# Optimization experiments

Hardware: AMD Instinct MI355X
Metric: run time of the kernel (lower is better)

Reference implementation:

```python
import jax, jax.numpy as jnp
import numpy as np

N = 1024      # num_features
H = 256       # num_hidden_features
E = 64        # embedding_size
HD = 64       # hidden_size
B = 8192


def setup_inputs() -> dict:
    key = jax.random.key(0)
    ks = jax.random.split(key, 7)
    glorot_e = (2.0 / (N + E)) ** 0.5
    glorot_w = (2.0 / (2 * E + HD)) ** 0.5
    glorot_u = (2.0 / (HD + 1)) ** 0.5
    return {
        "values": jax.random.uniform(ks[0], (B, N), dtype=jnp.float32),
        "feat_emb": jax.random.normal(ks[1], (N, E), dtype=jnp.float32) * glorot_e,
        "hid_emb": jax.random.normal(ks[2], (H, E), dtype=jnp.float32) * glorot_e,
        "W_w": jax.random.normal(ks[3], (2 * E, HD), dtype=jnp.float32) * glorot_w,
        "b_w": jnp.zeros((HD,), dtype=jnp.float32),
        "W_u": jax.random.normal(ks[4], (HD, 1), dtype=jnp.float32) * glorot_u,
        "mask": jax.random.bernoulli(ks[5], 0.5, (N, N + H)),
    }


def _forward(values, feat_emb, hid_emb, W_w, b_w, W_u, mask):
    # full embedding table over extended vocab: [M, E], M = N + H
    full = jnp.concatenate([feat_emb, hid_emb], axis=0)
    # Dense w applied to concat([feat_i, full_j]) == split-matmul, avoids [N,M,2E]
    W1, W2 = W_w[:E], W_w[E:]                      # each [E, HD]
    a = feat_emb @ W1                              # [N, HD]
    b = full @ W2                                  # [M, HD]
    h = jnp.tanh(a[:, None, :] + b[None, :, :] + b_w)  # [N, M, HD]
    score = jnp.squeeze(h @ W_u, axis=-1)          # [N, M]
    score = jnp.where(mask, jnp.exp(score), 0.0)
    score_sum = jnp.sum(score, axis=1, keepdims=True)
    score_sum = jnp.where(score_sum == 0, 1.0, score_sum)
    attention_weights = score / score_sum          # [N, M]
    context = attention_weights @ full             # [N, E]
    return values @ context                        # [B, E]


def reference(values, feat_emb, hid_emb, W_w, b_w, W_u, mask):
    return _forward(values, feat_emb, hid_emb, W_w, b_w, W_u, mask)
```

## Files before the change

kernel.cpp:

```cpp
#include <hip/hip_runtime.h>
#include <hip/hip_bf16.h>

#define NF   1024
#define NHID 256
#define NJ   1280
#define ED   64
#define BATCH 8192
#define SCB  320

#if defined(__has_builtin) && __has_builtin(__builtin_amdgcn_exp2f)
#define EXP2(x) __builtin_amdgcn_exp2f(x)
#else
#define EXP2(x) exp2f(x)
#endif
#define K2E 2.8853900817779268f

__global__ __launch_bounds__(256) void prep_kernel(
    const float* __restrict__ feat, const float* __restrict__ hid,
    const float* __restrict__ Ww, const float* __restrict__ bw,
    float* __restrict__ A, float* __restrict__ BvT)
{
    __shared__ float tile[32][65];
    const int tid = threadIdx.x;
    const int e   = tid & 63;
    const int wv  = tid >> 6;
    const int r0  = blockIdx.x * 32;
    const bool isA = (r0 < NF);
    const float* W = isA ? Ww : (Ww + 64 * 64);

    float wcol[64];
    #pragma unroll
    for (int k = 0; k < 64; k++) wcol[k] = W[k * 64 + e];
    const float bias = isA ? 0.f : bw[e];

    #pragma unroll
    for (int rr = 0; rr < 8; rr++) {
        int r  = r0 + wv * 8 + rr;
        int jf = isA ? r : (r - NF);
        jf = __builtin_amdgcn_readfirstlane(jf);
        const float* in = (jf < NF) ? (feat + (size_t)jf * 64)
                                    : (hid  + (size_t)(jf - NF) * 64);
        float a0 = 0.f, a1 = 0.f, a2 = 0.f, a3 = 0.f;
        #pragma unroll
        for (int k4 = 0; k4 < 64; k4 += 16) {
            float4 q0 = *(const float4*)(in + k4);
            float4 q1 = *(const float4*)(in + k4 + 4);
            float4 q2 = *(const float4*)(in + k4 + 8);
            float4 q3 = *(const float4*)(in + k4 + 12);
            a0 += q0.x*wcol[k4+0] + q0.y*wcol[k4+1] + q0.z*wcol[k4+2] + q0.w*wcol[k4+3];
            a1 += q1.x*wcol[k4+4] + q1.y*wcol[k4+5] + q1.z*wcol[k4+6] + q1.w*wcol[k4+7];
            a2 += q2.x*wcol[k4+8] + q2.y*wcol[k4+9] + q2.z*wcol[k4+10]+ q2.w*wcol[k4+11];
            a3 += q3.x*wcol[k4+12]+ q3.y*wcol[k4+13]+ q3.z*wcol[k4+14]+ q3.w*wcol[k4+15];
        }
        float res = (a0 + a1) + (a2 + a3) + bias;
        if (isA) A[(size_t)r * 64 + e] = res;
        else     tile[wv * 8 + rr][e] = res;
    }
    if (!isA) {
        __syncthreads();
        const int j0 = r0 - NF;
        const int ee = tid >> 2;
        #pragma unroll
        for (int h = 0; h < 2; h++) {
            int c = (tid & 3) + h * 4;
            float4 v;
            v.x = tile[c * 4 + 0][ee];
            v.y = tile[c * 4 + 1][ee];
            v.z = tile[c * 4 + 2][ee];
            v.w = tile[c * 4 + 3][ee];
            *(float4*)&BvT[(size_t)ee * NJ + j0 + c * 4] = v;
        }
    }
}

__global__ __launch_bounds__(SCB) void score_ctx_kernel(
    const float* __restrict__ feat, const float* __restrict__ hid,
    const float* __restrict__ Wu, const float* __restrict__ A,
    const float* __restrict__ BvT, const void* __restrict__ maskp,
    float* __restrict__ ctx)
{
    __shared__ __align__(16) float4 sPack[64];
    __shared__ __align__(16) float sc0[NJ], sc1[NJ];
    __shared__ __align__(16) float red[2][20][64];
    __shared__ float wpart[2][5];
    __shared__ float ssum[2];
    __shared__ float sSwu;
    __shared__ int   mtype_s;

    const int tid = threadIdx.x;
    const int i0  = blockIdx.x * 2;

    if (tid < 64) {
        const unsigned int* mw = (const unsigned int*)maskp;
        unsigned int w = mw[tid];
        unsigned long long notf = __ballot(w != 0u && w != 0x3F800000u);
        unsigned long long gt1  = __ballot(w > 1u);
        if (tid == 0) mtype_s = (notf == 0ull) ? 2 : ((gt1 == 0ull) ? 1 : 0);
        float wu = Wu[tid];
        float4 p;
        p.x = A[(size_t)i0 * 64 + tid];
        p.y = A[(size_t)(i0 + 1) * 64 + tid];
        p.z = wu; p.w = 0.f;
        sPack[tid] = p;
        float s = wu;
        #pragma unroll
        for (int off = 32; off > 0; off >>= 1) s += __shfl_down(s, off);
        if (tid == 0) sSwu = s;
    }
    __syncthreads();

    const int j4 = tid * 4;
    float4 acc0 = {0.f,0.f,0.f,0.f};
    float4 acc1 = {0.f,0.f,0.f,0.f};
    #pragma unroll 4
    for (int e = 0; e < 64; e++) {
        float4 b = *(const float4*)(BvT + (size_t)e * NJ + j4);
        float4 p = sPack[e];
        float x, r;
        x = p.x + b.x; r = __builtin_amdgcn_rcpf(EXP2(x * K2E) + 1.f); acc0.x = fmaf(p.z, r, acc0.x);
        x = p.x + b.y; r = __builtin_amdgcn_rcpf(EXP2(x * K2E) + 1.f); acc0.y = fmaf(p.z, r, acc0.y);
        x = p.x + b.z; r = __builtin_amdgcn_rcpf(EXP2(x * K2E) + 1.f); acc0.z = fmaf(p.z, r, acc0.z);
        x = p.x + b.w; r = __builtin_amdgcn_rcpf(EXP2(x * K2E) + 1.f); acc0.w = fmaf(p.z, r, acc0.w);
        x = p.y + b.x; r = __builtin_amdgcn_rcpf(EXP2(x * K2E) + 1.f); acc1.x = fmaf(p.z, r, acc1.x);
        x = p.y + b.y; r = __builtin_amdgcn_rcpf(EXP2(x * K2E) + 1.f); acc1.y = fmaf(p.z, r, acc1.y);
        x = p.y + b.z; r = __builtin_amdgcn_rcpf(EXP2(x * K2E) + 1.f); acc1.z = fmaf(p.z, r, acc1.z);
        x = p.y + b.w; r = __builtin_amdgcn_rcpf(EXP2(x * K2E) + 1.f); acc1.w = fmaf(p.z, r, acc1.w);
    }
    const float Swu = sSwu;
    const int mtype = mtype_s;
    const unsigned char* m8  = (const unsigned char*)maskp;
    const unsigned int*  m32 = (const unsigned int*)maskp;
    const float*         mfl = (const float*)maskp;
    bool b00,b01,b02,b03, b10,b11,b12,b13;
    if (mtype == 0) {
        unsigned m0 = *(const unsigned*)(m8 + (size_t)i0 * NJ + j4);
        unsigned m1 = *(const unsigned*)(m8 + (size_t)(i0+1) * NJ + j4);
        b00 = m0 & 0xffu; b01 = m0 & 0xff00u; b02 = m0 & 0xff0000u; b03 = m0 & 0xff000000u;
        b10 = m1 & 0xffu; b11 = m1 & 0xff00u; b12 = m1 & 0xff0000u; b13 = m1 & 0xff000000u;
    } else if (mtype == 1) {
        uint4 m0 = *(const uint4*)(m32 + (size_t)i0 * NJ + j4);
        uint4 m1 = *(const uint4*)(m32 + (size_t)(i0+1) * NJ + j4);
        b00 = m0.x; b01 = m0.y; b02 = m0.z; b03 = m0.w;
        b10 = m1.x; b11 = m1.y; b12 = m1.z; b13 = m1.w;
    } else {
        float4 m0 = *(const float4*)(mfl + (size_t)i0 * NJ + j4);
        float4 m1 = *(const float4*)(mfl + (size_t)(i0+1) * NJ + j4);
        b00 = m0.x != 0.f; b01 = m0.y != 0.f; b02 = m0.z != 0.f; b03 = m0.w != 0.f;
        b10 = m1.x != 0.f; b11 = m1.y != 0.f; b12 = m1.z != 0.f; b13 = m1.w != 0.f;
    }
    float4 e0, e1;
    e0.x = b00 ? __expf(Swu - 2.f*acc0.x) : 0.f;
    e0.y = b01 ? __expf(Swu - 2.f*acc0.y) : 0.f;
    e0.z = b02 ? __expf(Swu - 2.f*acc0.z) : 0.f;
    e0.w = b03 ? __expf(Swu - 2.f*acc0.w) : 0.f;
    e1.x = b10 ? __expf(Swu - 2.f*acc1.x) : 0.f;
    e1.y = b11 ? __expf(Swu - 2.f*acc1.y) : 0.f;
    e1.z = b12 ? __expf(Swu - 2.f*acc1.z) : 0.f;
    e1.w = b13 ? __expf(Swu - 2.f*acc1.w) : 0.f;
    *(float4*)&sc0[j4] = e0;
    *(float4*)&sc1[j4] = e1;
    float lsum0 = (e0.x + e0.y) + (e0.z + e0.w);
    float lsum1 = (e1.x + e1.y) + (e1.z + e1.w);
    #pragma unroll
    for (int off = 32; off > 0; off >>= 1) {
        lsum0 += __shfl_down(lsum0, off);
        lsum1 += __shfl_down(lsum1, off);
    }
    if ((tid & 63) == 0) { wpart[0][tid >> 6] = lsum0; wpart[1][tid >> 6] = lsum1; }
    __syncthreads();
    if (tid < 2) {
        float s = wpart[tid][0] + wpart[tid][1] + wpart[tid][2] + wpart[tid][3] + wpart[tid][4];
        ssum[tid] = (s == 0.f) ? 1.f : s;
    }
    __syncthreads();

    const int jg = tid >> 4;
    const int e4 = (tid & 15) * 4;
    float4 c0 = {0.f,0.f,0.f,0.f}, c1 = {0.f,0.f,0.f,0.f};
    for (int it = 0; it < 64; it++) {
        int j = it * 20 + jg;
        const float* fr = (j < NF) ? (feat + (size_t)j * 64)
                                   : (hid  + (size_t)(j - NF) * 64);
        float4 f = *(const float4*)(fr + e4);
        float w0 = sc0[j], w1 = sc1[j];
        c0.x += w0*f.x; c0.y += w0*f.y; c0.z += w0*f.z; c0.w += w0*f.w;
        c1.x += w1*f.x; c1.y += w1*f.y; c1.z += w1*f.z; c1.w += w1*f.w;
    }
    *(float4*)&red[0][jg][e4] = c0;
    *(float4*)&red[1][jg][e4] = c1;
    __syncthreads();
    if (tid < 128) {
        int half = tid >> 6, e = tid & 63;
        float v = 0.f;
        #pragma unroll
        for (int g = 0; g < 20; g++) v += red[half][g][e];
        ctx[(size_t)(i0 + half) * 64 + e] = v / ssum[half];
    }
}

__global__ __launch_bounds__(256) void out_mm_kernel(
    const float* __restrict__ values, const float* __restrict__ ctxp,
    float* __restrict__ dst, int atomic_mode)
{
    __shared__ __align__(16) float vsT[64 * 64];
    __shared__ __align__(16) float cs[64][64];
    const int tid = threadIdx.x;
    const int rt  = blockIdx.x >> 2;
    const int kq  = blockIdx.x & 3;
    const int r0  = rt * 64;
    const int tr  = tid >> 4;
    const int tc4 = (tid & 15) * 4;

    float acc[4][4];
    #pragma unroll
    for (int a = 0; a < 4; a++)
        #pragma unroll
        for (int b = 0; b < 4; b++) acc[a][b] = 0.f;

    for (int ch = 0; ch < 4; ch++) {
        const int k0 = kq * 256 + ch * 64;
        __syncthreads();
        #pragma unroll
        for (int s = 0; s < 4; s++) {
            int t   = tid + s * 256;
            int r   = t >> 4;
            int kk4 = (t & 15) * 4;
            float4 g = *(const float4*)&values[(size_t)(r0 + r) * NF + k0 + kk4];
            int p  = (((r >> 2) + (t & 15)) & 15) * 4 + (r & 3);
            vsT[(kk4 + 0) * 64 + p] = g.x;
            vsT[(kk4 + 1) * 64 + p] = g.y;
            vsT[(kk4 + 2) * 64 + p] = g.z;
            vsT[(kk4 + 3) * 64 + p] = g.w;
        }
        #pragma unroll
        for (int s = 0; s < 4; s++) {
            int t  = tid + s * 256;
            int kk = t >> 4;
            int c4 = (t & 15) * 4;
            *(float4*)&cs[kk][c4] = *(const float4*)&ctxp[(size_t)(k0 + kk) * ED + c4];
        }
        __syncthreads();
        #pragma unroll 8
        for (int k = 0; k < 64; k++) {
            float4 av = *(const float4*)&vsT[k * 64 + (((tr + (k >> 2)) & 15) << 2)];
            float4 bv = *(const float4*)&cs[k][tc4];
            acc[0][0] += av.x*bv.x; acc[0][1] += av.x*bv.y; acc[0][2] += av.x*bv.z; acc[0][3] += av.x*bv.w;
            acc[1][0] += av.y*bv.x; acc[1][1] += av.y*bv.y; acc[1][2] += av.y*bv.z; acc[1][3] += av.y*bv.w;
            acc[2][0] += av.z*bv.x; acc[2][1] += av.z*bv.y; acc[2][2] += av.z*bv.z; acc[2][3] += av.z*bv.w;
            acc[3][0] += av.w*bv.x; acc[3][1] += av.w*bv.y; acc[3][2] += av.w*bv.z; acc[3][3] += av.w*bv.w;
        }
    }
    if (atomic_mode) {
        #pragma unroll
        for (int i2 = 0; i2 < 4; i2++) {
            int r = r0 + tr * 4 + i2;
            float* op = dst + (size_t)r * ED + tc4;
            unsafeAtomicAdd(op + 0, acc[i2][0]);
            unsafeAtomicAdd(op + 1, acc[i2][1]);
            unsafeAtomicAdd(op + 2, acc[i2][2]);
            unsafeAtomicAdd(op + 3, acc[i2][3]);
        }
    } else {
        #pragma unroll
        for (int i2 = 0; i2 < 4; i2++) {
            int r = r0 + tr * 4 + i2;
            float* op = dst + ((size_t)kq * BATCH + r) * ED + tc4;
            *(float4*)op = make_float4(acc[i2][0], acc[i2][1], acc[i2][2], acc[i2][3]);
        }
    }
}

__global__ __launch_bounds__(256) void reduce4_kernel(
    const float* __restrict__ part, float* __restrict__ out)
{
    const size_t S = (size_t)BATCH * ED / 4;
    size_t idx = (size_t)blockIdx.x * 256 + threadIdx.x;
    const float4* p = (const float4*)part;
    float4 a = p[idx], b = p[idx + S], c = p[idx + 2*S], d = p[idx + 3*S];
    float4 r;
    r.x = (a.x + b.x) + (c.x + d.x);
    r.y = (a.y + b.y) + (c.y + d.y);
    r.z = (a.z + b.z) + (c.z + d.z);
    r.w = (a.w + b.w) + (c.w + d.w);
    ((float4*)out)[idx] = r;
}

extern "C" void kernel_launch(void* const* d_in, const int* in_sizes, int n_in,
                              void* d_out, int out_size, void* d_ws, size_t ws_size,
                              hipStream_t stream) {
    const float* values = (const float*)d_in[0];
    const float* feat   = (const float*)d_in[1];
    const float* hid    = (const float*)d_in[2];
    const float* Ww     = (const float*)d_in[3];
    const float* bw     = (const float*)d_in[4];
    const float* Wu     = (const float*)d_in[5];
    const void*  mask   = d_in[6];
    float* out = (float*)d_out;

    float* A    = (float*)d_ws;
    float* BvT  = A + (size_t)NF * 64;
    float* ctx  = BvT + (size_t)ED * NJ;
    float* part = ctx + (size_t)NF * 64;
    const size_t need = ((size_t)NF*64 + (size_t)ED*NJ + (size_t)NF*64
                         + (size_t)4*BATCH*ED) * sizeof(float);
    const bool wsmode = ws_size >= need;

    hipLaunchKernelGGL(prep_kernel, dim3((NF + NJ) / 32), dim3(256), 0, stream,
                       feat, hid, Ww, bw, A, BvT);
    hipLaunchKernelGGL(score_ctx_kernel, dim3(NF / 2), dim3(SCB), 0, stream,
                       feat, hid, Wu, A, BvT, mask, ctx);
    if (wsmode) {
        hipLaunchKernelGGL(out_mm_kernel, dim3(512), dim3(256), 0, stream,
                           values, ctx, part, 0);
        hipLaunchKernelGGL(reduce4_kernel, dim3(BATCH * ED / 4 / 256), dim3(256), 0, stream,
                           part, out);
    } else {
        hipMemsetAsync(d_out, 0, (size_t)BATCH * ED * sizeof(float), stream);
        hipLaunchKernelGGL(out_mm_kernel, dim3(512), dim3(256), 0, stream,
                           values, ctx, out, 1);
    }
}
```

Measured before the change: 148.2 us.

## Retile prep, score, and output kernels for more rows per block and split-K

The prep kernel now stages 64 input rows in shared memory and has each thread compute 16 rows, using 36 blocks instead of 72. The score/context kernel processes 4 query rows per block with 640 threads, each handling 2 columns, so it launches half as many blocks. The output matmul switches to 8-way split-K with 1024 blocks and an 8-way reduction. This trades fewer, larger blocks in the score phase for more parallelism in the output GEMM, at the cost of doubling the partial-sum traffic.

```diff
diff --git a/kernel.cpp b/kernel.cpp
--- a/kernel.cpp
+++ b/kernel.cpp
@@ -6,7 +6,7 @@
 #define NJ   1280
 #define ED   64
 #define BATCH 8192
-#define SCB  320
+#define SCB  640
 
 #if defined(__has_builtin) && __has_builtin(__builtin_amdgcn_exp2f)
 #define EXP2(x) __builtin_amdgcn_exp2f(x)
@@ -20,55 +20,57 @@
     const float* __restrict__ Ww, const float* __restrict__ bw,
     float* __restrict__ A, float* __restrict__ BvT)
 {
-    __shared__ float tile[32][65];
+    __shared__ __align__(16) float in_s[64][64];
+    __shared__ __align__(16) float tout[64][65];
     const int tid = threadIdx.x;
-    const int e   = tid & 63;
-    const int wv  = tid >> 6;
-    const int r0  = blockIdx.x * 32;
-    const bool isA = (r0 < NF);
-    const float* W = isA ? Ww : (Ww + 64 * 64);
-
+    const int b   = blockIdx.x;
+    const bool isA = (b < 16);
+    const int e  = tid & 63;
+    const int wv = tid >> 6;
+
+    const float* W = isA ? Ww : (Ww + 4096);
     float wcol[64];
     #pragma unroll
     for (int k = 0; k < 64; k++) wcol[k] = W[k * 64 + e];
     const float bias = isA ? 0.f : bw[e];
 
-    #pragma unroll
-    for (int rr = 0; rr < 8; rr++) {
-        int r  = r0 + wv * 8 + rr;
-        int jf = isA ? r : (r - NF);
-        jf = __builtin_amdgcn_readfirstlane(jf);
-        const float* in = (jf < NF) ? (feat + (size_t)jf * 64)
-                                    : (hid  + (size_t)(jf - NF) * 64);
-        float a0 = 0.f, a1 = 0.f, a2 = 0.f, a3 = 0.f;
-        #pragma unroll
-        for (int k4 = 0; k4 < 64; k4 += 16) {
-            float4 q0 = *(const float4*)(in + k4);
-            float4 q1 = *(const float4*)(in + k4 + 4);
-            float4 q2 = *(const float4*)(in + k4 + 8);
-            float4 q3 = *(const float4*)(in + k4 + 12);
-            a0 += q0.x*wcol[k4+0] + q0.y*wcol[k4+1] + q0.z*wcol[k4+2] + q0.w*wcol[k4+3];
-            a1 += q1.x*wcol[k4+4] + q1.y*wcol[k4+5] + q1.z*wcol[k4+6] + q1.w*wcol[k4+7];
-            a2 += q2.x*wcol[k4+8] + q2.y*wcol[k4+9] + q2.z*wcol[k4+10]+ q2.w*wcol[k4+11];
-            a3 += q3.x*wcol[k4+12]+ q3.y*wcol[k4+13]+ q3.z*wcol[k4+14]+ q3.w*wcol[k4+15];
-        }
-        float res = (a0 + a1) + (a2 + a3) + bias;
-        if (isA) A[(size_t)r * 64 + e] = res;
-        else     tile[wv * 8 + rr][e] = res;
-    }
-    if (!isA) {
+    const int bb = isA ? b : (b - 16);
+    const float* src = isA ? (feat + (size_t)bb * 4096)
+                     : (bb < 16 ? (feat + (size_t)bb * 4096)
+                                : (hid + (size_t)(bb - 16) * 4096));
+    #pragma unroll
+    for (int s = 0; s < 4; s++)
+        ((float4*)&in_s[0][0])[tid + s * 256] = ((const float4*)src)[tid + s * 256];
+    __syncthreads();
+
+    float acc[16];
+    #pragma unroll
+    for (int r = 0; r < 16; r++) acc[r] = bias;
+    for (int k4 = 0; k4 < 64; k4 += 4) {
+        #pragma unroll
+        for (int r = 0; r < 16; r++) {
+            float4 iv = *(const float4*)&in_s[wv * 16 + r][k4];
+            acc[r] += iv.x*wcol[k4+0] + iv.y*wcol[k4+1] + iv.z*wcol[k4+2] + iv.w*wcol[k4+3];
+        }
+    }
+
+    if (isA) {
+        #pragma unroll
+        for (int r = 0; r < 16; r++)
+            A[(size_t)(b * 64 + wv * 16 + r) * 64 + e] = acc[r];
+    } else {
+        #pragma unroll
+        for (int r = 0; r < 16; r++) tout[wv * 16 + r][e] = acc[r];
         __syncthreads();
-        const int j0 = r0 - NF;
-        const int ee = tid >> 2;
-        #pragma unroll
-        for (int h = 0; h < 2; h++) {
-            int c = (tid & 3) + h * 4;
+        const int j0 = bb * 64;
+        #pragma unroll
+        for (int q = 0; q < 4; q++) {
             float4 v;
-            v.x = tile[c * 4 + 0][ee];
-            v.y = tile[c * 4 + 1][ee];
-            v.z = tile[c * 4 + 2][ee];
-            v.w = tile[c * 4 + 3][ee];
-            *(float4*)&BvT[(size_t)ee * NJ + j0 + c * 4] = v;
+            v.x = tout[wv * 16 + q * 4 + 0][e];
+            v.y = tout[wv * 16 + q * 4 + 1][e];
+            v.z = tout[wv * 16 + q * 4 + 2][e];
+            v.w = tout[wv * 16 + q * 4 + 3][e];
+            *(float4*)&BvT[(size_t)e * NJ + j0 + wv * 16 + q * 4] = v;
         }
     }
 }
@@ -79,16 +81,17 @@
     const float* __restrict__ BvT, const void* __restrict__ maskp,
     float* __restrict__ ctx)
 {
-    __shared__ __align__(16) float4 sPack[64];
-    __shared__ __align__(16) float sc0[NJ], sc1[NJ];
-    __shared__ __align__(16) float red[2][20][64];
-    __shared__ float wpart[2][5];
-    __shared__ float ssum[2];
+    __shared__ __align__(16) float4 sA4[64];
+    __shared__ __align__(16) float  sWu[64];
+    __shared__ __align__(16) float  sc[4][NJ];
+    __shared__ __align__(16) float  red[4][40][64];
+    __shared__ float wpart[4][10];
+    __shared__ float ssum[4];
     __shared__ float sSwu;
     __shared__ int   mtype_s;
 
     const int tid = threadIdx.x;
-    const int i0  = blockIdx.x * 2;
+    const int i0  = blockIdx.x * 4;
 
     if (tid < 64) {
         const unsigned int* mw = (const unsigned int*)maskp;
@@ -98,10 +101,12 @@
         if (tid == 0) mtype_s = (notf == 0ull) ? 2 : ((gt1 == 0ull) ? 1 : 0);
         float wu = Wu[tid];
         float4 p;
-        p.x = A[(size_t)i0 * 64 + tid];
+        p.x = A[(size_t)(i0 + 0) * 64 + tid];
         p.y = A[(size_t)(i0 + 1) * 64 + tid];
-        p.z = wu; p.w = 0.f;
-        sPack[tid] = p;
+        p.z = A[(size_t)(i0 + 2) * 64 + tid];
+        p.w = A[(size_t)(i0 + 3) * 64 + tid];
+        sA4[tid] = p;
+        sWu[tid] = wu;
         float s = wu;
         #pragma unroll
         for (int off = 32; off > 0; off >>= 1) s += __shfl_down(s, off);
@@ -109,91 +114,98 @@
     }
     __syncthreads();
 
-    const int j4 = tid * 4;
-    float4 acc0 = {0.f,0.f,0.f,0.f};
-    float4 acc1 = {0.f,0.f,0.f,0.f};
+    const int j2 = tid * 2;
+    float2 acc[4];
+    #pragma unroll
+    for (int i = 0; i < 4; i++) acc[i] = make_float2(0.f, 0.f);
+
     #pragma unroll 4
     for (int e = 0; e < 64; e++) {
-        float4 b = *(const float4*)(BvT + (size_t)e * NJ + j4);
-        float4 p = sPack[e];
+        float2 b = *(const float2*)(BvT + (size_t)e * NJ + j2);
+        float4 p = sA4[e];
+        float wu = sWu[e];
         float x, r;
-        x = p.x + b.x; r = __builtin_amdgcn_rcpf(EXP2(x * K2E) + 1.f); acc0.x = fmaf(p.z, r, acc0.x);
-        x = p.x + b.y; r = __builtin_amdgcn_rcpf(EXP2(x * K2E) + 1.f); acc0.y = fmaf(p.z, r, acc0.y);
-        x = p.x + b.z; r = __builtin_amdgcn_rcpf(EXP2(x * K2E) + 1.f); acc0.z = fmaf(p.z, r, acc0.z);
-        x = p.x + b.w; r = __builtin_amdgcn_rcpf(EXP2(x * K2E) + 1.f); acc0.w = fmaf(p.z, r, acc0.w);
-        x = p.y + b.x; r = __builtin_amdgcn_rcpf(EXP2(x * K2E) + 1.f); acc1.x = fmaf(p.z, r, acc1.x);
-        x = p.y + b.y; r = __builtin_amdgcn_rcpf(EXP2(x * K2E) + 1.f); acc1.y = fmaf(p.z, r, acc1.y);
-        x = p.y + b.z; r = __builtin_amdgcn_rcpf(EXP2(x * K2E) + 1.f); acc1.z = fmaf(p.z, r, acc1.z);
-        x = p.y + b.w; r = __builtin_amdgcn_rcpf(EXP2(x * K2E) + 1.f); acc1.w = fmaf(p.z, r, acc1.w);
-    }
+        x = p.x + b.x; r = __builtin_amdgcn_rcpf(EXP2(x*K2E) + 1.f); acc[0].x = fmaf(wu, r, acc[0].x);
+        x = p.x + b.y; r = __builtin_amdgcn_rcpf(EXP2(x*K2E) + 1.f); acc[0].y = fmaf(wu, r, acc[0].y);
+        x = p.y + b.x; r = __builtin_amdgcn_rcpf(EXP2(x*K2E) + 1.f); acc[1].x = fmaf(wu, r, acc[1].x);
+        x = p.y + b.y; r = __builtin_amdgcn_rcpf(EXP2(x*K2E) + 1.f); acc[1].y = fmaf(wu, r, acc[1].y);
+        x = p.z + b.x; r = __builtin_amdgcn_rcpf(EXP2(x*K2E) + 1.f); acc[2].x = fmaf(wu, r, acc[2].x);
+        x = p.z + b.y; r = __builtin_amdgcn_rcpf(EXP2(x*K2E) + 1.f); acc[2].y = fmaf(wu, r, acc[2].y);
+        x = p.w + b.x; r = __builtin_amdgcn_rcpf(EXP2(x*K2E) + 1.f); acc[3].x = fmaf(wu, r, acc[3].x);
+        x = p.w + b.y; r = __builtin_amdgcn_rcpf(EXP2(x*K2E) + 1.f); acc[3].y = fmaf(wu, r, acc[3].y);
+    }
+
     const float Swu = sSwu;
     const int mtype = mtype_s;
     const unsigned char* m8  = (const unsigned char*)maskp;
     const unsigned int*  m32 = (const unsigned int*)maskp;
     const float*         mfl = (const float*)maskp;
-    bool b00,b01,b02,b03, b10,b11,b12,b13;
-    if (mtype == 0) {
-        unsigned m0 = *(const unsigned*)(m8 + (size_t)i0 * NJ + j4);
-        unsigned m1 = *(const unsigned*)(m8 + (size_t)(i0+1) * NJ + j4);
-        b00 = m0 & 0xffu; b01 = m0 & 0xff00u; b02 = m0 & 0xff0000u; b03 = m0 & 0xff000000u;
-        b10 = m1 & 0xffu; b11 = m1 & 0xff00u; b12 = m1 & 0xff0000u; b13 = m1 & 0xff000000u;
-    } else if (mtype == 1) {
-        uint4 m0 = *(const uint4*)(m32 + (size_t)i0 * NJ + j4);
-        uint4 m1 = *(const uint4*)(m32 + (size_t)(i0+1) * NJ + j4);
-        b00 = m0.x; b01 = m0.y; b02 = m0.z; b03 = m0.w;
-        b10 = m1.x; b11 = m1.y; b12 = m1.z; b13 = m1.w;
-    } else {
-        float4 m0 = *(const float4*)(mfl + (size_t)i0 * NJ + j4);
-        float4 m1 = *(const float4*)(mfl + (size_t)(i0+1) * NJ + j4);
-        b00 = m0.x != 0.f; b01 = m0.y != 0.f; b02 = m0.z != 0.f; b03 = m0.w != 0.f;
-        b10 = m1.x != 0.f; b11 = m1.y != 0.f; b12 = m1.z != 0.f; b13 = m1.w != 0.f;
-    }
-    float4 e0, e1;
-    e0.x = b00 ? __expf(Swu - 2.f*acc0.x) : 0.f;
-    e0.y = b01 ? __expf(Swu - 2.f*acc0.y) : 0.f;
-    e0.z = b02 ? __expf(Swu - 2.f*acc0.z) : 0.f;
-    e0.w = b03 ? __expf(Swu - 2.f*acc0.w) : 0.f;
-    e1.x = b10 ? __expf(Swu - 2.f*acc1.x) : 0.f;
-    e1.y = b11 ? __expf(Swu - 2.f*acc1.y) : 0.f;
-    e1.z = b12 ? __expf(Swu - 2.f*acc1.z) : 0.f;
-    e1.w = b13 ? __expf(Swu - 2.f*acc1.w) : 0.f;
-    *(float4*)&sc0[j4] = e0;
-    *(float4*)&sc1[j4] = e1;
-    float lsum0 = (e0.x + e0.y) + (e0.z + e0.w);
-    float lsum1 = (e1.x + e1.y) + (e1.z + e1.w);
+
+    float lsum[4];
+    #pragma unroll
+    for (int i = 0; i < 4; i++) {
+        size_t off = (size_t)(i0 + i) * NJ + j2;
+        bool b0, b1;
+        if (mtype == 0) {
+            unsigned short m = *(const unsigned short*)(m8 + off);
+            b0 = (m & 0xffu) != 0; b1 = (m >> 8) != 0;
+        } else if (mtype == 1) {
+            uint2 m = *(const uint2*)(m32 + off);
+            b0 = m.x != 0u; b1 = m.y != 0u;
+        } else {
+            float2 m = *(const float2*)(mfl + off);
+            b0 = m.x != 0.f; b1 = m.y != 0.f;
+        }
+        float e0 = b0 ? __expf(Swu - 2.f * acc[i].x) : 0.f;
+        float e1 = b1 ? __expf(Swu - 2.f * acc[i].y) : 0.f;
+        *(float2*)&sc[i][j2] = make_float2(e0, e1);
+        lsum[i] = e0 + e1;
+    }
     #pragma unroll
     for (int off = 32; off > 0; off >>= 1) {
-        lsum0 += __shfl_down(lsum0, off);
-        lsum1 += __shfl_down(lsum1, off);
-    }
-    if ((tid & 63) == 0) { wpart[0][tid >> 6] = lsum0; wpart[1][tid >> 6] = lsum1; }
-    __syncthreads();
-    if (tid < 2) {
-        float s = wpart[tid][0] + wpart[tid][1] + wpart[tid][2] + wpart[tid][3] + wpart[tid][4];
+        lsum[0] += __shfl_down(lsum[0], off);
+        lsum[1] += __shfl_down(lsum[1], off);
+        lsum[2] += __shfl_down(lsum[2], off);
+        lsum[3] += __shfl_down(lsum[3], off);
+    }
+    if ((tid & 63) == 0) {
+        int wv = tid >> 6;
+        wpart[0][wv] = lsum[0]; wpart[1][wv] = lsum[1];
+        wpart[2][wv] = lsum[2]; wpart[3][wv] = lsum[3];
+    }
+    __syncthreads();
+    if (tid < 4) {
+        float s = 0.f;
+        #pragma unroll
+        for (int g = 0; g < 10; g++) s += wpart[tid][g];
         ssum[tid] = (s == 0.f) ? 1.f : s;
     }
     __syncthreads();
 
     const int jg = tid >> 4;
     const int e4 = (tid & 15) * 4;
-    float4 c0 = {0.f,0.f,0.f,0.f}, c1 = {0.f,0.f,0.f,0.f};
-    for (int it = 0; it < 64; it++) {
-        int j = it * 20 + jg;
+    float4 c[4];
+    #pragma unroll
+    for (int i = 0; i < 4; i++) c[i] = make_float4(0.f, 0.f, 0.f, 0.f);
+    for (int it = 0; it < 32; it++) {
+        int j = it * 40 + jg;
         const float* fr = (j < NF) ? (feat + (size_t)j * 64)
                                    : (hid  + (size_t)(j - NF) * 64);
         float4 f = *(const float4*)(fr + e4);
-        float w0 = sc0[j], w1 = sc1[j];
-        c0.x += w0*f.x; c0.y += w0*f.y; c0.z += w0*f.z; c0.w += w0*f.w;
-        c1.x += w1*f.x; c1.y += w1*f.y; c1.z += w1*f.z; c1.w += w1*f.w;
-    }
-    *(float4*)&red[0][jg][e4] = c0;
-    *(float4*)&red[1][jg][e4] = c1;
-    __syncthreads();
-    if (tid < 128) {
+        #pragma unroll
+        for (int i = 0; i < 4; i++) {
+            float w = sc[i][j];
+            c[i].x += w*f.x; c[i].y += w*f.y; c[i].z += w*f.z; c[i].w += w*f.w;
+        }
+    }
+    #pragma unroll
+    for (int i = 0; i < 4; i++) *(float4*)&red[i][jg][e4] = c[i];
+    __syncthreads();
+    if (tid < 256) {
         int half = tid >> 6, e = tid & 63;
         float v = 0.f;
         #pragma unroll
-        for (int g = 0; g < 20; g++) v += red[half][g][e];
+        for (int g = 0; g < 40; g++) v += red[half][g][e];
         ctx[(size_t)(i0 + half) * 64 + e] = v / ssum[half];
     }
 }
@@ -205,8 +217,8 @@
     __shared__ __align__(16) float vsT[64 * 64];
     __shared__ __align__(16) float cs[64][64];
     const int tid = threadIdx.x;
-    const int rt  = blockIdx.x >> 2;
-    const int kq  = blockIdx.x & 3;
+    const int rt  = blockIdx.x >> 3;
+    const int kq  = blockIdx.x & 7;
     const int r0  = rt * 64;
     const int tr  = tid >> 4;
     const int tc4 = (tid & 15) * 4;
@@ -217,8 +229,8 @@
         #pragma unroll
         for (int b = 0; b < 4; b++) acc[a][b] = 0.f;
 
-    for (int ch = 0; ch < 4; ch++) {
-        const int k0 = kq * 256 + ch * 64;
+    for (int ch = 0; ch < 2; ch++) {
+        const int k0 = kq * 128 + ch * 64;
         __syncthreads();
         #pragma unroll
         for (int s = 0; s < 4; s++) {
@@ -270,18 +282,18 @@
     }
 }
 
-__global__ __launch_bounds__(256) void reduce4_kernel(
+__global__ __launch_bounds__(256) void reduce8_kernel(
     const float* __restrict__ part, float* __restrict__ out)
 {
     const size_t S = (size_t)BATCH * ED / 4;
     size_t idx = (size_t)blockIdx.x * 256 + threadIdx.x;
     const float4* p = (const float4*)part;
-    float4 a = p[idx], b = p[idx + S], c = p[idx + 2*S], d = p[idx + 3*S];
-    float4 r;
-    r.x = (a.x + b.x) + (c.x + d.x);
-    r.y = (a.y + b.y) + (c.y + d.y);
-    r.z = (a.z + b.z) + (c.z + d.z);
-    r.w = (a.w + b.w) + (c.w + d.w);
+    float4 r = {0.f, 0.f, 0.f, 0.f};
+    #pragma unroll
+    for (int q = 0; q < 8; q++) {
+        float4 a = p[idx + (size_t)q * S];
+        r.x += a.x; r.y += a.y; r.z += a.z; r.w += a.w;
+    }
     ((float4*)out)[idx] = r;
 }
 
@@ -302,21 +314,21 @@
     float* ctx  = BvT + (size_t)ED * NJ;
     float* part = ctx + (size_t)NF * 64;
     const size_t need = ((size_t)NF*64 + (size_t)ED*NJ + (size_t)NF*64
-                         + (size_t)4*BATCH*ED) * sizeof(float);
+                         + (size_t)8*BATCH*ED) * sizeof(float);
     const bool wsmode = ws_size >= need;
 
-    hipLaunchKernelGGL(prep_kernel, dim3((NF + NJ) / 32), dim3(256), 0, stream,
+    hipLaunchKernelGGL(prep_kernel, dim3(36), dim3(256), 0, stream,
                        feat, hid, Ww, bw, A, BvT);
-    hipLaunchKernelGGL(score_ctx_kernel, dim3(NF / 2), dim3(SCB), 0, stream,
+    hipLaunchKernelGGL(score_ctx_kernel, dim3(NF / 4), dim3(SCB), 0, stream,
                        feat, hid, Wu, A, BvT, mask, ctx);
     if (wsmode) {
-        hipLaunchKernelGGL(out_mm_kernel, dim3(512), dim3(256), 0, stream,
+        hipLaunchKernelGGL(out_mm_kernel, dim3(1024), dim3(256), 0, stream,
                            values, ctx, part, 0);
-        hipLaunchKernelGGL(reduce4_kernel, dim3(BATCH * ED / 4 / 256), dim3(256), 0, stream,
+        hipLaunchKernelGGL(reduce8_kernel, dim3(BATCH * ED / 4 / 256), dim3(256), 0, stream,
                            part, out);
     } else {
         hipMemsetAsync(d_out, 0, (size_t)BATCH * ED * sizeof(float), stream);
-        hipLaunchKernelGGL(out_mm_kernel, dim3(512), dim3(256), 0, stream,
+        hipLaunchKernelGGL(out_mm_kernel, dim3(1024), dim3(256), 0, stream,
                            values, ctx, out, 1);
     }
 }
```

Measured after the change: 172.9 us. 1.17x slower.
